# Kernel optimization log

Measured on AMD Instinct MI355X. Metric: run time of the kernel, lower is better.

Reference implementation:

```python
import jax, jax.numpy as jnp
import numpy as np

E = 512      # embedding_dim == head_dim
H = 8        # num_heads
F = E * H    # ffn_dim = 4096
B = 2
S = 2048
SCALE = float(np.sqrt(E))


def setup_inputs() -> dict:
    key = jax.random.key(0)
    kx, kq, kk, kv, ko = jax.random.split(key, 5)
    x = jax.random.normal(kx, (B, S, E), dtype=jnp.float32)
    # torch Linear weights: [out_features, in_features], y = x @ W.T
    w_std = 1.0 / np.sqrt(E)
    Wq = jax.random.normal(kq, (F, E), dtype=jnp.float32) * w_std
    Wk = jax.random.normal(kk, (F, E), dtype=jnp.float32) * w_std
    Wv = jax.random.normal(kv, (F, E), dtype=jnp.float32) * w_std
    Wo = jax.random.normal(ko, (E, F), dtype=jnp.float32) * (1.0 / np.sqrt(F))
    # causal mask: 1 where attended, 0 where masked (masked_fill(mask == 0, -inf))
    attn_mask = jnp.tril(jnp.ones((S, S), dtype=jnp.int32))[None, None]  # [1,1,S,S]
    return {"x": x, "attn_mask": attn_mask, "Wq": Wq, "Wk": Wk, "Wv": Wv, "Wo": Wo}


def reference(x, attn_mask, Wq, Wk, Wv, Wo):
    b, s, _ = x.shape
    # projections + split heads: [B,S,F] -> [B,S,H,E]
    q = (x @ Wq.T).reshape(b, s, H, E)
    k = (x @ Wk.T).reshape(b, s, H, E)
    v = (x @ Wv.T).reshape(b, s, H, E)
    # scaled dot-product scores [B,H,S,S]
    scores = jnp.einsum('bqhd,bkhd->bhqk', q, k) / SCALE
    scores = jnp.where(attn_mask == 0, -jnp.inf, scores)
    w = jax.nn.softmax(scores, axis=-1)
    # dropout rate 0.0 (eval) -> identity
    out = jnp.einsum('bhqk,bkhd->bqhd', w, v).reshape(b, s, F)
    return out @ Wo.T  # [B,S,E]
```

## Files before the change

### kernel.cpp

```cpp
#include <hip/hip_runtime.h>
#include <hip/hip_bf16.h>

typedef __attribute__((ext_vector_type(8))) short short8;
typedef __attribute__((ext_vector_type(4))) float f32x4;
typedef __attribute__((ext_vector_type(8))) unsigned short ushort8;

#define LDS_ASYNC16(gsrc, ldst) \
  __builtin_amdgcn_global_load_lds((const __attribute__((address_space(1))) void*)(gsrc), \
                                   (__attribute__((address_space(3))) void*)(ldst), 16, 0, 0)

__device__ __forceinline__ unsigned short f2bf(float f) {
  unsigned int u = __float_as_uint(f);
  unsigned int r = (u + 0x7FFFu + ((u >> 16) & 1u)) >> 16;
  return (unsigned short)r;
}
__device__ __forceinline__ float bf2f(unsigned short h) {
  return __uint_as_float((unsigned int)h << 16);
}

__global__ __launch_bounds__(256) void cast5_f32_bf16(
    const float* __restrict__ i0, const float* __restrict__ i1, const float* __restrict__ i2,
    const float* __restrict__ i3, const float* __restrict__ i4,
    unsigned short* __restrict__ out) {
  const float* src[5] = {i0, i1, i2, i3, i4};
  int z = blockIdx.z;
  const float* in = src[z];
  size_t i = ((size_t)blockIdx.x * 256 + threadIdx.x) * 8;
  float4 a = *(const float4*)(in + i);
  float4 b = *(const float4*)(in + i + 4);
  ushort8 o;
  o[0] = f2bf(a.x); o[1] = f2bf(a.y); o[2] = f2bf(a.z); o[3] = f2bf(a.w);
  o[4] = f2bf(b.x); o[5] = f2bf(b.y); o[6] = f2bf(b.z); o[7] = f2bf(b.w);
  *(ushort8*)(out + (size_t)z * 2097152 + i) = o;
}

__global__ __launch_bounds__(256) void transpose_v(const unsigned short* __restrict__ V,
                                                   unsigned short* __restrict__ Vt) {
  __shared__ unsigned short t[64][72];
  int slot = blockIdx.z;
  int k0 = blockIdx.x << 6, d0 = blockIdx.y << 6;
  const unsigned short* src = V + (size_t)k0 * 4096 + slot * 512 + d0;
  int rr = threadIdx.x >> 3;
  int cc = (threadIdx.x & 7) << 3;
#pragma unroll
  for (int half = 0; half < 64; half += 32) {
    int r = rr + half;
    ushort8 v = *(const ushort8*)(src + (size_t)r * 4096 + cc);
#pragma unroll
    for (int e = 0; e < 8; ++e) t[cc + e][r] = v[e];
  }
  __syncthreads();
  unsigned short* dst = Vt + ((size_t)slot * 512 + d0) * 2048 + k0;
#pragma unroll
  for (int half = 0; half < 64; half += 32) {
    int d = rr + half;
    *(ushort8*)(dst + (size_t)d * 2048 + cc) = *(const ushort8*)&t[d][cc];
  }
}

__global__ __launch_bounds__(256) void softmax_causal_bf16(unsigned short* __restrict__ S) {
  int row = blockIdx.x;
  int q = row & 2047;
  unsigned short* srow = S + (size_t)row * 2048;
  int n = q + 1;
  int nW = ((q >> 7) + 1) << 7;
  int t = threadIdx.x, wave = t >> 6, lane = t & 63;
  int base = t * 8;
  ushort8 u = {};
  if (base < nW) u = *(const ushort8*)(srow + base);
  float vals[8];
  float m = -1e30f;
#pragma unroll
  for (int e = 0; e < 8; ++e) {
    float v = bf2f(u[e]);
    vals[e] = (base + e < n) ? v : -1e30f;
    m = fmaxf(m, vals[e]);
  }
#pragma unroll
  for (int off = 32; off > 0; off >>= 1) m = fmaxf(m, __shfl_xor(m, off, 64));
  __shared__ float red[8];
  if (lane == 0) red[wave] = m;
  __syncthreads();
  m = fmaxf(fmaxf(red[0], red[1]), fmaxf(red[2], red[3]));
  float s = 0.f;
#pragma unroll
  for (int e = 0; e < 8; ++e) {
    float ex = (base + e < n) ? __expf(vals[e] - m) : 0.f;
    vals[e] = ex; s += ex;
  }
#pragma unroll
  for (int off = 32; off > 0; off >>= 1) s += __shfl_xor(s, off, 64);
  if (lane == 0) red[4 + wave] = s;
  __syncthreads();
  s = red[4] + red[5] + red[6] + red[7];
  float inv = 1.0f / s;
  if (base < nW) {
    ushort8 o;
#pragma unroll
    for (int e = 0; e < 8; ++e) o[e] = f2bf(vals[e] * inv);
    *(ushort8*)(srow + base) = o;
  }
}

__global__ __launch_bounds__(256) void reduce_k4(const float4* __restrict__ p,
                                                 float4* __restrict__ out, int n4) {
  int i = blockIdx.x * 256 + threadIdx.x;
  if (i >= n4) return;
  float4 a = p[i], b = p[i + n4], c = p[i + 2 * n4], d = p[i + 3 * n4];
  float4 o;
  o.x = (a.x + b.x) + (c.x + d.x);
  o.y = (a.y + b.y) + (c.y + d.y);
  o.z = (a.z + b.z) + (c.z + d.z);
  o.w = (a.w + b.w) + (c.w + d.w);
  out[i] = o;
}

#define STGU(u_)                                                                   \
  do {                                                                             \
    int kb_ = (u_) * 32;                                                           \
    unsigned short* Ad_ = AsBase + ((u_) & 3) * 8192 + tid * 8;                    \
    unsigned short* Bd_ = BsBase + ((u_) & 3) * 8192 + tid * 8;                    \
    LDS_ASYNC16(Ap + (size_t)(m0 + r0) * lda + kb_ + cs0, Ad_);                    \
    LDS_ASYNC16(Bp + (size_t)(n0 + r0) * ldb + kb_ + cs0, Bd_);                    \
    LDS_ASYNC16(Ap + (size_t)(m0 + r0 + 128) * lda + kb_ + cs0, Ad_ + 4096);       \
    LDS_ASYNC16(Bp + (size_t)(n0 + r0 + 128) * ldb + kb_ + cs0, Bd_ + 4096);       \
  } while (0)

#define RDFR(u_, AF, BF)                                                           \
  {                                                                                \
    const unsigned short* Au_ = AsBase + ((u_) & 3) * 8192;                        \
    const unsigned short* Bu_ = BsBase + ((u_) & 3) * 8192;                        \
    _Pragma("unroll") for (int j_ = 0; j_ < 8; ++j_)                               \
      AF[j_] = *(const short8*)(Au_ + (wm * 128 + j_ * 16 + lr) * 32 + sA);        \
    _Pragma("unroll") for (int j_ = 0; j_ < 4; ++j_)                               \
      BF[j_] = *(const short8*)(Bu_ + (wn * 64 + j_ * 16 + lr) * 32 + sA);         \
  }

#define MMAC(AF, BF)                                                               \
  __builtin_amdgcn_s_setprio(1);                                                   \
  _Pragma("unroll") for (int j_ = 0; j_ < 8; ++j_)                                 \
    _Pragma("unroll") for (int j2_ = 0; j2_ < 4; ++j2_)                            \
      acc[j_][j2_] = __builtin_amdgcn_mfma_f32_16x16x32_bf16(AF[j_], BF[j2_],      \
                                                             acc[j_][j2_], 0, 0, 0); \
  __builtin_amdgcn_s_setprio(0);

#define VMC4() asm volatile("s_waitcnt vmcnt(4)" ::: "memory")
#define VMC0() asm volatile("s_waitcnt vmcnt(0)" ::: "memory")
#define VMC8() asm volatile("s_waitcnt vmcnt(8)" ::: "memory")
#define BARR() __builtin_amdgcn_s_barrier()

template<int OUT_F32, int CSKIP>
__global__ __launch_bounds__(512, 2) void gemm8p(
    const unsigned short* __restrict__ A, const unsigned short* __restrict__ B,
    void* __restrict__ C, int K , int lda, int ldb, int ldc, int nH,
    long long sAb, long long sAh, long long sBb, long long sBh,
    long long sCb, long long sCh, float scale)
{
  __shared__ unsigned short AsBase[4 * 8192];
  __shared__ unsigned short BsBase[4 * 8192];
  int m0 = blockIdx.y * 256, n0 = blockIdx.x * 256;
  if (CSKIP && n0 > m0) return;
  int z = blockIdx.z;
  int zb = z / nH, zh = z - zb * nH;
  const unsigned short* Ap = A + (size_t)(zb * sAb + zh * sAh);
  const unsigned short* Bp = B + (size_t)(zb * sBb + zh * sBh);
  size_t coff = (size_t)(zb * sCb + zh * sCh);
  int tid = threadIdx.x;
  int wid = tid >> 6, lane = tid & 63;
  int wm = wid >> 2, wn = wid & 3;
  int lr = lane & 15, hi = lane >> 4;
  int sA  = (hi ^ ((lr >> 1) & 3)) << 3;
  int r0  = tid >> 2;
  int cs0 = ((tid & 3) ^ ((r0 >> 1) & 3)) << 3;

  short8 af0[8], bf0[4], af1[8], bf1[4];
  f32x4 acc[8][4] = {};

  STGU(0); STGU(1); STGU(2);
  VMC8(); BARR();
  RDFR(0, af0, bf0);
  VMC4(); BARR();

  for (int u = 0; u < 12; u += 2) {
    RDFR(u + 1, af1, bf1); STGU(u + 3); MMAC(af0, bf0); VMC4(); BARR();
    RDFR(u + 2, af0, bf0); STGU(u + 4); MMAC(af1, bf1); VMC4(); BARR();
  }
  RDFR(13, af1, bf1); STGU(15); MMAC(af0, bf0); VMC4(); BARR();
  RDFR(14, af0, bf0);           MMAC(af1, bf1); VMC0(); BARR();
  RDFR(15, af1, bf1);           MMAC(af0, bf0);         BARR();
                                MMAC(af1, bf1);

#pragma unroll
  for (int m = 0; m < 8; ++m)
#pragma unroll
    for (int n = 0; n < 4; ++n)
#pragma unroll
      for (int r = 0; r < 4; ++r) {
        int row = m0 + wm * 128 + m * 16 + hi * 4 + r;
        int col = n0 + wn * 64 + n * 16 + lr;
        float v = acc[m][n][r] * scale;
        if (OUT_F32) ((float*)C)[coff + (size_t)row * ldc + col] = v;
        else ((unsigned short*)C)[coff + (size_t)row * ldc + col] = f2bf(v);
      }
}

template<int OUT_F32, int CSKIP, int KCLIP>
__global__ __launch_bounds__(256, 2) void gemm_bt(
    const unsigned short* __restrict__ A, const unsigned short* __restrict__ B,
    void* __restrict__ C, int K, int lda, int ldb, int ldc, int nH,
    long long sAb, long long sAh, long long sBb, long long sBh,
    long long sCb, long long sCh, float scale)
{
  __shared__ unsigned short As[128 * 64];
  __shared__ unsigned short Bs[128 * 64];
  int m0 = blockIdx.y * 128, n0 = blockIdx.x * 128;
  if (CSKIP && n0 > m0) return;
  int z = blockIdx.z;
  int zb = z / nH, zh = z - zb * nH;
  const unsigned short* Ap = A + (size_t)(zb * sAb + zh * sAh);
  const unsigned short* Bp = B + (size_t)(zb * sBb + zh * sBh);
  size_t coff = (size_t)(zb * sCb + zh * sCh);
  int tid = threadIdx.x;
  int wave = tid >> 6, lane = tid & 63;
  int kEnd = KCLIP ? min(K, m0 + 128) : K;

  int wr = (wave >> 1) * 64, wc = (wave & 1) * 64;
  int lr = lane & 15;
  int lkb = (lane >> 4) * 8;

  f32x4 acc[4][4] = {};

  for (int k0 = 0; k0 < kEnd; k0 += 64) {
#pragma unroll
    for (int it = 0; it < 4; ++it) {
      int g = it * 256 + tid;
      int r = g >> 3, c = (g & 7) << 3;
      LDS_ASYNC16(Ap + (size_t)(m0 + r) * lda + (k0 + c), As + (size_t)(it * 256 + wave * 64) * 8);
      LDS_ASYNC16(Bp + (size_t)(n0 + r) * ldb + (k0 + c), Bs + (size_t)(it * 256 + wave * 64) * 8);
    }
    __syncthreads();
#pragma unroll
    for (int kk = 0; kk < 64; kk += 32) {
      short8 a[4], b[4];
#pragma unroll
      for (int i = 0; i < 4; ++i)
        a[i] = *(const short8*)(As + (size_t)(wr + i * 16 + lr) * 64 + kk + lkb);
#pragma unroll
      for (int j = 0; j < 4; ++j)
        b[j] = *(const short8*)(Bs + (size_t)(wc + j * 16 + lr) * 64 + kk + lkb);
#pragma unroll
      for (int i = 0; i < 4; ++i)
#pragma unroll
        for (int j = 0; j < 4; ++j)
          acc[i][j] = __builtin_amdgcn_mfma_f32_16x16x32_bf16(a[i], b[j], acc[i][j], 0, 0, 0);
    }
    __syncthreads();
  }

  int orow = (lane >> 4) * 4, ocol = lane & 15;
#pragma unroll
  for (int i = 0; i < 4; ++i)
#pragma unroll
    for (int j = 0; j < 4; ++j)
#pragma unroll
      for (int r = 0; r < 4; ++r) {
        int row = m0 + wr + i * 16 + orow + r;
        int col = n0 + wc + j * 16 + ocol;
        float v = acc[i][j][r] * scale;
        if (OUT_F32) ((float*)C)[coff + (size_t)row * ldc + col] = v;
        else ((unsigned short*)C)[coff + (size_t)row * ldc + col] = f2bf(v);
      }
}

extern "C" void kernel_launch(void* const* d_in, const int* in_sizes, int n_in,
                              void* d_out, int out_size, void* d_ws, size_t ws_size,
                              hipStream_t stream) {
  const float* x  = (const float*)d_in[0];
  const float* Wq = (const float*)d_in[2];
  const float* Wk = (const float*)d_in[3];
  const float* Wv = (const float*)d_in[4];
  const float* Wo = (const float*)d_in[5];

  if (ws_size < (size_t)188 * (1 << 20)) return;

  char* ws = (char*)d_ws;
  unsigned short* xb   = (unsigned short*)(ws);
  unsigned short* Wob  = (unsigned short*)(ws + (size_t)16  * (1 << 20));
  unsigned short* QKV  = (unsigned short*)(ws + (size_t)20  * (1 << 20));
  unsigned short* Sc   = (unsigned short*)(ws + (size_t)116 * (1 << 20));
  unsigned short* Vt   = (unsigned short*)(ws);
  float*          Pp   = (float*)(ws + (size_t)116 * (1 << 20));

  const int NEw = 4096 * 512;
  const long long NEm = 4096LL * 4096;

  cast5_f32_bf16<<<dim3(1024, 1, 5), 256, 0, stream>>>(x, Wq, Wk, Wv, Wo, xb);

  gemm8p<0, 0><<<dim3(16, 16, 3), 512, 0, stream>>>(
      xb, xb + NEw, QKV, 512, 512, 512, 4096, 3,
      0LL, 0LL, 0LL, (long long)NEw, 0LL, NEm, 1.0f);

  for (int b = 0; b < 2; ++b) {
    size_t tokOff = (size_t)b * 2048 * 4096;
    const unsigned short* Qb = QKV + tokOff;
    const unsigned short* Kb = QKV + NEm + tokOff;
    const unsigned short* Vb = QKV + 2 * NEm + tokOff;
    unsigned short* AOb = QKV + tokOff;

    gemm8p<0, 1><<<dim3(8, 8, 8), 512, 0, stream>>>(
        Qb, Kb, Sc, 512, 4096, 4096, 2048, 8,
        0LL, 512LL, 0LL, 512LL, 0LL, 2048LL * 2048, 0.04419417382415922f);

    transpose_v<<<dim3(32, 8, 8), 256, 0, stream>>>(Vb, Vt);

    softmax_causal_bf16<<<dim3(8 * 2048), 256, 0, stream>>>(Sc);

    gemm_bt<0, 0, 1><<<dim3(4, 16, 8), 256, 0, stream>>>(
        Sc, Vt, AOb, 2048, 2048, 2048, 4096, 8,
        0LL, 2048LL * 2048, 0LL, 512LL * 2048, 0LL, 512LL, 1.0f);
  }

  gemm_bt<1, 0, 0><<<dim3(4, 32, 4), 256, 0, stream>>>(
      QKV, Wob, Pp, 1024, 4096, 4096, 512, 4,
      0LL, 1024LL, 0LL, 1024LL, 0LL, 2097152LL, 1.0f);

  reduce_k4<<<dim3(2048), 256, 0, stream>>>((const float4*)Pp, (float4*)d_out, 524288);
}
```

Measured before the change: 339.9 us.

## Fuse softmax into score GEMM epilogue and PV GEMM prologue via partial row stats

Removes the standalone causal softmax pass over the score matrix. The QK^T GEMM epilogue now applies the causal mask, scales by log2e/sqrt(d), and writes per-64-column partial (max, sum-of-exp2) stats. A tiny merge kernel combines these into a row max and inverse sum, and the PV GEMM normalizes scores on the fly while loading A (exp2, scale, convert to bf16) instead of using async LDS loads. It also reverses the row-block order for some heads to balance the causal work. This saves one full read/write of the scores, at the cost of extra ALU work and synchronous A loads in the PV GEMM.

After: 414.4 us. 21.9% more time.

```diff
diff --git a/kernel.cpp b/kernel.cpp
--- a/kernel.cpp
+++ b/kernel.cpp
@@ -58,48 +58,18 @@
   }
 }
 
-__global__ __launch_bounds__(256) void softmax_causal_bf16(unsigned short* __restrict__ S) {
-  int row = blockIdx.x;
-  int q = row & 2047;
-  unsigned short* srow = S + (size_t)row * 2048;
-  int n = q + 1;
-  int nW = ((q >> 7) + 1) << 7;
-  int t = threadIdx.x, wave = t >> 6, lane = t & 63;
-  int base = t * 8;
-  ushort8 u = {};
-  if (base < nW) u = *(const ushort8*)(srow + base);
-  float vals[8];
-  float m = -1e30f;
-#pragma unroll
-  for (int e = 0; e < 8; ++e) {
-    float v = bf2f(u[e]);
-    vals[e] = (base + e < n) ? v : -1e30f;
-    m = fmaxf(m, vals[e]);
-  }
-#pragma unroll
-  for (int off = 32; off > 0; off >>= 1) m = fmaxf(m, __shfl_xor(m, off, 64));
-  __shared__ float red[8];
-  if (lane == 0) red[wave] = m;
-  __syncthreads();
-  m = fmaxf(fmaxf(red[0], red[1]), fmaxf(red[2], red[3]));
-  float s = 0.f;
-#pragma unroll
-  for (int e = 0; e < 8; ++e) {
-    float ex = (base + e < n) ? __expf(vals[e] - m) : 0.f;
-    vals[e] = ex; s += ex;
-  }
-#pragma unroll
-  for (int off = 32; off > 0; off >>= 1) s += __shfl_xor(s, off, 64);
-  if (lane == 0) red[4 + wave] = s;
-  __syncthreads();
-  s = red[4] + red[5] + red[6] + red[7];
-  float inv = 1.0f / s;
-  if (base < nW) {
-    ushort8 o;
-#pragma unroll
-    for (int e = 0; e < 8; ++e) o[e] = f2bf(vals[e] * inv);
-    *(ushort8*)(srow + base) = o;
-  }
+__global__ __launch_bounds__(256) void merge_stats(const float2* __restrict__ ss,
+                                                   float2* __restrict__ rs) {
+  int i = blockIdx.x * 256 + threadIdx.x;
+  int z = i >> 11, row = i & 2047;
+  int nks = (row >> 6) + 1;
+  float m = -1e30f, l = 0.f;
+  for (int ks = 0; ks < nks; ++ks) {
+    float2 p = ss[((size_t)z * 32 + ks) * 2048 + row];
+    if (p.x > m) { l = l * exp2f(m - p.x) + p.y; m = p.x; }
+    else l += p.y * exp2f(p.x - m);
+  }
+  rs[i] = make_float2(m, 1.0f / l);
 }
 
 __global__ __launch_bounds__(256) void reduce_k4(const float4* __restrict__ p,
@@ -149,12 +119,12 @@
 #define VMC8() asm volatile("s_waitcnt vmcnt(8)" ::: "memory")
 #define BARR() __builtin_amdgcn_s_barrier()
 
-template<int OUT_F32, int CSKIP>
+template<int OUT_F32, int CSKIP, int STATS>
 __global__ __launch_bounds__(512, 2) void gemm8p(
     const unsigned short* __restrict__ A, const unsigned short* __restrict__ B,
     void* __restrict__ C, int K , int lda, int ldb, int ldc, int nH,
     long long sAb, long long sAh, long long sBb, long long sBh,
-    long long sCb, long long sCh, float scale)
+    long long sCb, long long sCh, float scale, float2* __restrict__ stats)
 {
   __shared__ unsigned short AsBase[4 * 8192];
   __shared__ unsigned short BsBase[4 * 8192];
@@ -191,29 +161,58 @@
                                 MMAC(af1, bf1);
 
 #pragma unroll
-  for (int m = 0; m < 8; ++m)
-#pragma unroll
-    for (int n = 0; n < 4; ++n)
-#pragma unroll
-      for (int r = 0; r < 4; ++r) {
+  for (int m = 0; m < 8; ++m) {
+#pragma unroll
+    for (int r = 0; r < 4; ++r) {
+      if (STATS) {
+        int rowl = wm * 128 + m * 16 + hi * 4 + r;
+        int grow = m0 + rowl;
+        float vs[4];
+        float vmax = -1e30f;
+#pragma unroll
+        for (int n = 0; n < 4; ++n) {
+          int gcol = n0 + wn * 64 + n * 16 + lr;
+          float v = acc[m][n][r] * scale;
+          if (gcol > grow) v = -1e30f;
+          acc[m][n][r] = v;
+          vs[n] = v; vmax = fmaxf(vmax, v);
+        }
+#pragma unroll
+        for (int off = 1; off < 16; off <<= 1) vmax = fmaxf(vmax, __shfl_xor(vmax, off, 64));
+        float s = 0.f;
+#pragma unroll
+        for (int n = 0; n < 4; ++n) s += exp2f(vs[n] - vmax);
+#pragma unroll
+        for (int off = 1; off < 16; off <<= 1) s += __shfl_xor(s, off, 64);
+        if (lr == 0) {
+          int ks = blockIdx.x * 4 + wn;
+          stats[((size_t)zh * 32 + ks) * 2048 + grow] = make_float2(vmax, s);
+        }
+      }
+#pragma unroll
+      for (int n = 0; n < 4; ++n) {
         int row = m0 + wm * 128 + m * 16 + hi * 4 + r;
         int col = n0 + wn * 64 + n * 16 + lr;
-        float v = acc[m][n][r] * scale;
+        float v = STATS ? acc[m][n][r] : acc[m][n][r] * scale;
         if (OUT_F32) ((float*)C)[coff + (size_t)row * ldc + col] = v;
         else ((unsigned short*)C)[coff + (size_t)row * ldc + col] = f2bf(v);
       }
-}
-
-template<int OUT_F32, int CSKIP, int KCLIP>
+    }
+  }
+}
+
+template<int OUT_F32, int CSKIP, int KCLIP, int TRANS_A>
 __global__ __launch_bounds__(256, 2) void gemm_bt(
     const unsigned short* __restrict__ A, const unsigned short* __restrict__ B,
     void* __restrict__ C, int K, int lda, int ldb, int ldc, int nH,
     long long sAb, long long sAh, long long sBb, long long sBh,
-    long long sCb, long long sCh, float scale)
+    long long sCb, long long sCh, float scale, const float2* __restrict__ rowstats)
 {
   __shared__ unsigned short As[128 * 64];
   __shared__ unsigned short Bs[128 * 64];
-  int m0 = blockIdx.y * 128, n0 = blockIdx.x * 128;
+  int by = blockIdx.y;
+  if (KCLIP && ((blockIdx.z >> 2) & 1)) by = gridDim.y - 1 - by;
+  int m0 = by * 128, n0 = blockIdx.x * 128;
   if (CSKIP && n0 > m0) return;
   int z = blockIdx.z;
   int zb = z / nH, zh = z - zb * nH;
@@ -228,6 +227,16 @@
   int lr = lane & 15;
   int lkb = (lane >> 4) * 8;
 
+  float rm[4], ri[4];
+  if (TRANS_A) {
+#pragma unroll
+    for (int it = 0; it < 4; ++it) {
+      int g = it * 256 + tid;
+      float2 s2 = rowstats[(size_t)zh * 2048 + (m0 + (g >> 3))];
+      rm[it] = s2.x; ri[it] = s2.y;
+    }
+  }
+
   f32x4 acc[4][4] = {};
 
   for (int k0 = 0; k0 < kEnd; k0 += 64) {
@@ -235,7 +244,16 @@
     for (int it = 0; it < 4; ++it) {
       int g = it * 256 + tid;
       int r = g >> 3, c = (g & 7) << 3;
-      LDS_ASYNC16(Ap + (size_t)(m0 + r) * lda + (k0 + c), As + (size_t)(it * 256 + wave * 64) * 8);
+      if (TRANS_A) {
+        ushort8 sv = *(const ushort8*)(Ap + (size_t)(m0 + r) * lda + (k0 + c));
+        ushort8 pv;
+#pragma unroll
+        for (int e = 0; e < 8; ++e)
+          pv[e] = f2bf(exp2f(bf2f(sv[e]) - rm[it]) * ri[it]);
+        *(ushort8*)(As + (size_t)g * 8) = pv;
+      } else {
+        LDS_ASYNC16(Ap + (size_t)(m0 + r) * lda + (k0 + c), As + (size_t)(it * 256 + wave * 64) * 8);
+      }
       LDS_ASYNC16(Bp + (size_t)(n0 + r) * ldb + (k0 + c), Bs + (size_t)(it * 256 + wave * 64) * 8);
     }
     __syncthreads();
@@ -290,15 +308,17 @@
   unsigned short* Sc   = (unsigned short*)(ws + (size_t)116 * (1 << 20));
   unsigned short* Vt   = (unsigned short*)(ws);
   float*          Pp   = (float*)(ws + (size_t)116 * (1 << 20));
+  float2*         Sst  = (float2*)(ws + (size_t)180 * (1 << 20));
+  float2*         Rst  = (float2*)(ws + (size_t)185 * (1 << 20));
 
   const int NEw = 4096 * 512;
   const long long NEm = 4096LL * 4096;
 
   cast5_f32_bf16<<<dim3(1024, 1, 5), 256, 0, stream>>>(x, Wq, Wk, Wv, Wo, xb);
 
-  gemm8p<0, 0><<<dim3(16, 16, 3), 512, 0, stream>>>(
+  gemm8p<0, 0, 0><<<dim3(16, 16, 3), 512, 0, stream>>>(
       xb, xb + NEw, QKV, 512, 512, 512, 4096, 3,
-      0LL, 0LL, 0LL, (long long)NEw, 0LL, NEm, 1.0f);
+      0LL, 0LL, 0LL, (long long)NEw, 0LL, NEm, 1.0f, nullptr);
 
   for (int b = 0; b < 2; ++b) {
     size_t tokOff = (size_t)b * 2048 * 4096;
@@ -307,22 +327,22 @@
     const unsigned short* Vb = QKV + 2 * NEm + tokOff;
     unsigned short* AOb = QKV + tokOff;
 
-    gemm8p<0, 1><<<dim3(8, 8, 8), 512, 0, stream>>>(
+    gemm8p<0, 1, 1><<<dim3(8, 8, 8), 512, 0, stream>>>(
         Qb, Kb, Sc, 512, 4096, 4096, 2048, 8,
-        0LL, 512LL, 0LL, 512LL, 0LL, 2048LL * 2048, 0.04419417382415922f);
+        0LL, 512LL, 0LL, 512LL, 0LL, 2048LL * 2048, 0.0637587213f, Sst);
 
     transpose_v<<<dim3(32, 8, 8), 256, 0, stream>>>(Vb, Vt);
 
-    softmax_causal_bf16<<<dim3(8 * 2048), 256, 0, stream>>>(Sc);
-
-    gemm_bt<0, 0, 1><<<dim3(4, 16, 8), 256, 0, stream>>>(
+    merge_stats<<<dim3(64), 256, 0, stream>>>(Sst, Rst);
+
+    gemm_bt<0, 0, 1, 1><<<dim3(4, 16, 8), 256, 0, stream>>>(
         Sc, Vt, AOb, 2048, 2048, 2048, 4096, 8,
-        0LL, 2048LL * 2048, 0LL, 512LL * 2048, 0LL, 512LL, 1.0f);
-  }
-
-  gemm_bt<1, 0, 0><<<dim3(4, 32, 4), 256, 0, stream>>>(
+        0LL, 2048LL * 2048, 0LL, 512LL * 2048, 0LL, 512LL, 1.0f, Rst);
+  }
+
+  gemm_bt<1, 0, 0, 0><<<dim3(4, 32, 4), 256, 0, stream>>>(
       QKV, Wob, Pp, 1024, 4096, 4096, 512, 4,
-      0LL, 1024LL, 0LL, 1024LL, 0LL, 2097152LL, 1.0f);
+      0LL, 1024LL, 0LL, 1024LL, 0LL, 2097152LL, 1.0f, nullptr);
 
   reduce_k4<<<dim3(2048), 256, 0, stream>>>((const float4*)Pp, (float4*)d_out, 524288);
 }
```
